# Optimization experiments

Measured on AMD Instinct MI355X. Metric: run time of the kernel, lower is better.

Reference implementation:

```python
import jax, jax.numpy as jnp
import numpy as np

B, D, L = 2, 1024, 4096   # batch, channels (= num_heads), seq len
FS = 4                    # filter_size
DEPTH = 11                # ceil(log2((L-1)/(FS-1)+1))
LN_EPS = 1e-5


def setup_inputs() -> dict:
    key = jax.random.key(0)
    ks = jax.random.split(key, 7)
    return {
        "x": jax.random.normal(ks[0], (B, D, L), jnp.float32),
        "h0": jax.random.normal(ks[1], (D, 1, FS), jnp.float32) * 0.2,
        "h1": jax.random.normal(ks[2], (D, 1, FS), jnp.float32) * 0.2,
        "w_mix": jax.random.normal(ks[3], (D, D), jnp.float32) / np.sqrt(D),
        "b_mix": jnp.zeros((D,), jnp.float32),
        "ln_gamma": jnp.ones((D,), jnp.float32),
        "ln_beta": jnp.zeros((D,), jnp.float32),
    }


def _dw_conv(a, h, dilation):
    # depthwise (groups = D) dilated conv1d, cross-correlation like torch
    return jax.lax.conv_general_dilated(
        a, h, window_strides=(1,), padding='VALID',
        rhs_dilation=(dilation,),
        dimension_numbers=('NCH', 'OIH', 'NCH'),
        feature_group_count=D)


def reference(x, h0, h1, w_mix, b_mix, ln_gamma, ln_beta):
    # --- multires conv tree ---
    a = x
    dilation = 1
    a_list, b_list = [], []
    for _ in range(DEPTH):
        pad = dilation * (FS - 1)
        ap = jnp.pad(a, ((0, 0), (0, 0), (pad, 0)))  # left causal pad
        b = _dw_conv(ap, h1, dilation)
        a = _dw_conv(ap, h0, dilation)
        a_list.append(a)
        b_list.append(b)
        dilation *= 2
    # --- gated combination across scales (deepest level first) ---
    a_rev = a_list[::-1]
    b_rev = b_list[::-1]
    y = jnp.zeros_like(x)
    gated = None
    for i in range(DEPTH):
        if i + 1 < DEPTH:
            gated = jax.nn.sigmoid(a_rev[i]) * b_rev[i + 1]
        # last iteration reuses the previous gated tensor (matches original)
        y = y + gated
    # --- 1x1 channel mix (Dropout1d is identity in eval) + residual ---
    mixed = jnp.einsum('oc,bcl->bol', w_mix, y) + b_mix[None, :, None]
    z = mixed + x
    # --- LayerNorm over channel dim ---
    mu = jnp.mean(z, axis=1, keepdims=True)
    var = jnp.mean(jnp.square(z - mu), axis=1, keepdims=True)
    out = (z - mu) * jax.lax.rsqrt(var + LN_EPS)
    out = out * ln_gamma[None, :, None] + ln_beta[None, :, None]
    return out
```

## Files before the change

### kernel.cpp

```cpp
#include <hip/hip_runtime.h>
#include <hip/hip_bf16.h>
#include <hip/hip_fp16.h>

#define NB 2
#define ND 1024
#define NL 4096
#define NFS 4
#define NDEPTH 11
#define LN_EPS 1e-5f

#define BM 128
#define BN 128
#define BK 32
#define NKI (ND / BK)
#define ASZ (BM * BK)

#define CPAD 3072
#define CBUF (CPAD + NL)

typedef __bf16 bf16x8 __attribute__((ext_vector_type(8)));
typedef float f32x4 __attribute__((ext_vector_type(4)));
typedef _Float16 half8 __attribute__((ext_vector_type(8)));

__device__ __forceinline__ unsigned short f2bf(float f) {
    __hip_bfloat16 h = __float2bfloat16(f);
    unsigned short u;
    __builtin_memcpy(&u, &h, 2);
    return u;
}

__device__ __forceinline__ float bf2f(unsigned short u) {
    unsigned int ui = (unsigned int)u << 16;
    float f;
    __builtin_memcpy(&f, &ui, 4);
    return f;
}

__device__ __forceinline__ unsigned int pack2bf(float lo, float hi) {
    return (unsigned int)f2bf(lo) | ((unsigned int)f2bf(hi) << 16);
}

__device__ __forceinline__ void llds16(const void* g, void* l) {
    __builtin_amdgcn_global_load_lds(
        (const __attribute__((address_space(1))) unsigned int*)g,
        (__attribute__((address_space(3))) unsigned int*)l, 16, 0, 0);
}

__global__ __launch_bounds__(256) void wconv_kernel(const float* __restrict__ w,
                                                    unsigned short* __restrict__ wbf) {
    const int idx8 = (blockIdx.x * 256 + threadIdx.x) * 8;
    const float4 v0 = *reinterpret_cast<const float4*>(w + idx8);
    const float4 v1 = *reinterpret_cast<const float4*>(w + idx8 + 4);
    uint4 o;
    o.x = pack2bf(v0.x, v0.y);
    o.y = pack2bf(v0.z, v0.w);
    o.z = pack2bf(v1.x, v1.y);
    o.w = pack2bf(v1.z, v1.w);
    *reinterpret_cast<uint4*>(wbf + idx8) = o;
}

__global__ __launch_bounds__(512, 8) void conv_cascade_kernel(const float* __restrict__ x,
                                                              const float* __restrict__ h0,
                                                              const float* __restrict__ h1,
                                                              unsigned short* __restrict__ ybf) {
    __shared__ _Float16 a_sh[2][CBUF];
    const int row = blockIdx.x;
    const int d = row & (ND - 1);
    const int t = threadIdx.x;

    if (t < CPAD / 8) {
        *reinterpret_cast<half8*>(&a_sh[0][t * 8]) = (half8)0;
        *reinterpret_cast<half8*>(&a_sh[1][t * 8]) = (half8)0;
    }

    const float* xrow = x + (size_t)row * NL;

    _Float16 h0c[NFS], h1c[NFS];
#pragma unroll
    for (int k = 0; k < NFS; ++k) {
        h0c[k] = (_Float16)h0[d * NFS + k];
        h1c[k] = (_Float16)h1[d * NFS + k];
    }

    const int A = CPAD + t * 8;
    half8 cur;
    {
        const float4 v0 = *reinterpret_cast<const float4*>(xrow + t * 8);
        const float4 v1 = *reinterpret_cast<const float4*>(xrow + t * 8 + 4);
        cur[0] = (_Float16)v0.x; cur[1] = (_Float16)v0.y;
        cur[2] = (_Float16)v0.z; cur[3] = (_Float16)v0.w;
        cur[4] = (_Float16)v1.x; cur[5] = (_Float16)v1.y;
        cur[6] = (_Float16)v1.z; cur[7] = (_Float16)v1.w;
    }
    _Float16* rbp = &a_sh[0][0];
    _Float16* wbp = &a_sh[1][0];
    *reinterpret_cast<half8*>(&rbp[A]) = cur;

    const __half2 nlog2e = __float2half2_rn(-1.44269504f);
    const __half2 one2 = __float2half2_rn(1.f);
    const __half2 two2 = __float2half2_rn(2.f);
    __half2 yacc2[4];
#pragma unroll
    for (int p = 0; p < 4; ++p) yacc2[p] = __float2half2_rn(0.f);
    half8 bprev = (half8)0;
    __syncthreads();

    half8 an, bn;

#define CMATH(a1, a2, a3)                                           \
    an = cur * h0c[3] + (a1)*h0c[2] + (a2)*h0c[1] + (a3)*h0c[0];    \
    bn = cur * h1c[3] + (a1)*h1c[2] + (a2)*h1c[1] + (a3)*h1c[0];

#define GATE(SC2)                                                   \
    {                                                               \
        __half2 ap[4], bp[4];                                       \
        __builtin_memcpy(ap, &an, 16);                              \
        __builtin_memcpy(bp, &bprev, 16);                           \
        _Pragma("unroll") for (int p = 0; p < 4; ++p) {             \
            const __half2 e = h2exp2(__hmul2(ap[p], nlog2e));       \
            const __half2 s = h2rcp(__hadd2(e, one2));              \
            const __half2 g = __hmul2(__hmul2(s, bp[p]), SC2);      \
            yacc2[p] = __hadd2(g, yacc2[p]);                        \
        }                                                           \
    }

#define CFIN()                                                      \
    {                                                               \
        *reinterpret_cast<half8*>(&wbp[A]) = an;                    \
        cur = an;                                                   \
        bprev = bn;                                                 \
        _Float16* tmpp = rbp; rbp = wbp; wbp = tmpp;                \
    }

    {
        const half8 m = *reinterpret_cast<const half8*>(&rbp[A - 8]);
        const half8 a1 = __builtin_shufflevector(m, cur, 7, 8, 9, 10, 11, 12, 13, 14);
        const half8 a2 = __builtin_shufflevector(m, cur, 6, 7, 8, 9, 10, 11, 12, 13);
        const half8 a3 = __builtin_shufflevector(m, cur, 5, 6, 7, 8, 9, 10, 11, 12);
        CMATH(a1, a2, a3)
        CFIN()
        __syncthreads();
    }

    {
        const half8 m = *reinterpret_cast<const half8*>(&rbp[A - 8]);
        const half8 a1 = __builtin_shufflevector(m, cur, 6, 7, 8, 9, 10, 11, 12, 13);
        const half8 a2 = __builtin_shufflevector(m, cur, 4, 5, 6, 7, 8, 9, 10, 11);
        const half8 a3 = __builtin_shufflevector(m, cur, 2, 3, 4, 5, 6, 7, 8, 9);
        CMATH(a1, a2, a3)
        GATE(two2)
        CFIN()
        __syncthreads();
    }

    {
        const half8 m = *reinterpret_cast<const half8*>(&rbp[A - 8]);
        const half8 m2 = *reinterpret_cast<const half8*>(&rbp[A - 16]);
        const half8 a1 = __builtin_shufflevector(m, cur, 4, 5, 6, 7, 8, 9, 10, 11);
        const half8 a3 = __builtin_shufflevector(m2, m, 4, 5, 6, 7, 8, 9, 10, 11);
        CMATH(a1, m, a3)
        GATE(one2)
        CFIN()
        __syncthreads();
    }

    int dil = 8;
#pragma unroll 1
    for (int lev = 3; lev <= 9; ++lev) {
        const half8 a1 = *reinterpret_cast<const half8*>(&rbp[A - dil]);
        const half8 a2 = *reinterpret_cast<const half8*>(&rbp[A - 2 * dil]);
        const half8 a3 = *reinterpret_cast<const half8*>(&rbp[A - 3 * dil]);
        CMATH(a1, a2, a3)
        GATE(one2)
        CFIN()
        dil <<= 1;
        __syncthreads();
    }

    {
        const half8 a1 = *reinterpret_cast<const half8*>(&rbp[A - 1024]);
        const half8 a2 = *reinterpret_cast<const half8*>(&rbp[A - 2048]);
        const half8 a3 = *reinterpret_cast<const half8*>(&rbp[A - 3072]);
        an = cur * h0c[3] + a1 * h0c[2] + a2 * h0c[1] + a3 * h0c[0];
        GATE(one2)
    }
#undef CMATH
#undef GATE
#undef CFIN

    const float2 f0 = __half22float2(yacc2[0]);
    const float2 f1 = __half22float2(yacc2[1]);
    const float2 f2 = __half22float2(yacc2[2]);
    const float2 f3 = __half22float2(yacc2[3]);
    uint4 o;
    o.x = pack2bf(f0.x, f0.y);
    o.y = pack2bf(f1.x, f1.y);
    o.z = pack2bf(f2.x, f2.y);
    o.w = pack2bf(f3.x, f3.y);
    *reinterpret_cast<uint4*>(ybf + (size_t)row * NL + t * 8) = o;
}

__global__ __launch_bounds__(256) void transpose_kernel(const unsigned short* __restrict__ ybf,
                                                        unsigned short* __restrict__ yT) {
    __shared__ unsigned short tile[64][66];
    const int l0 = blockIdx.x * 64;
    const int c0 = blockIdx.y * 64;
    const int b = blockIdx.z;
    const int t = threadIdx.x;
    const int li = t & 63, cg = t >> 6;
#pragma unroll
    for (int k = 0; k < 16; ++k) {
        const int ci = cg * 16 + k;
        tile[ci][li] = ybf[(size_t)(b * ND + c0 + ci) * NL + l0 + li];
    }
    __syncthreads();
    const int ci2 = t & 63, lg = t >> 6;
#pragma unroll
    for (int k = 0; k < 16; ++k) {
        const int li2 = lg * 16 + k;
        yT[((size_t)b * NL + l0 + li2) * ND + c0 + ci2] = tile[ci2][li2];
    }
}

__global__ __launch_bounds__(256) void gemm_kernel(const unsigned short* __restrict__ wbf,
                                                   const unsigned short* __restrict__ yT,
                                                   const float* __restrict__ bmix,
                                                   unsigned short* __restrict__ mixed) {
    __shared__ unsigned short As[3][BM][BK];
    __shared__ unsigned short Bs[3][BN][BK];

    const int orig = blockIdx.x;
    const int wgid = (orig & 7) * 64 + (orig >> 3);
    const int b = wgid & 1;
    const int m0 = ((wgid >> 1) & 7) * BM;
    const int n0 = (wgid >> 4) * BN;

    const int t = threadIdx.x;
    const int lane = t & 63, wid = t >> 6;
    const int wr = wid >> 1, wc = wid & 1;
    const int fr = lane & 15;
    const int fk = (lane >> 4) * 8;

    const int srow = wid * 32 + (lane >> 2);
    const int sk = (lane & 3) * 8;
    const unsigned short* Ag = wbf + (size_t)(m0 + srow) * ND + sk;
    const unsigned short* Bg = yT + ((size_t)b * NL + n0 + srow) * ND + sk;
    unsigned short* A0 = &As[0][0][0];
    unsigned short* B0 = &Bs[0][0][0];
    unsigned short* AsW = A0 + wid * 32 * BK;
    unsigned short* BsW = B0 + wid * 32 * BK;

#define STAGE(bo, kt)                           \
    llds16(Ag + (kt), AsW + (bo));              \
    llds16(Ag + (kt) + 16 * ND, AsW + (bo) + 16 * BK); \
    llds16(Bg + (kt), BsW + (bo));              \
    llds16(Bg + (kt) + 16 * ND, BsW + (bo) + 16 * BK);

    f32x4 acc[4][4];
#pragma unroll
    for (int mi = 0; mi < 4; ++mi)
#pragma unroll
        for (int ni = 0; ni < 4; ++ni)
            acc[mi][ni] = (f32x4){0.f, 0.f, 0.f, 0.f};

    STAGE(0, 0)
    STAGE(ASZ, BK)

    int bc = 0;
    int bs = 2;
#pragma unroll 1
    for (int ki = 0; ki < NKI; ++ki) {
        if (ki + 1 < NKI) {
            asm volatile("s_waitcnt vmcnt(4)" ::: "memory");
        } else {
            asm volatile("s_waitcnt vmcnt(0)" ::: "memory");
        }
        __builtin_amdgcn_s_barrier();
        __builtin_amdgcn_sched_barrier(0);

        if (ki + 2 < NKI) {
            const int bo = bs * ASZ;
            const int kt = (ki + 2) * BK;
            STAGE(bo, kt)
        }

        const int bco = bc * ASZ;
        bf16x8 af[4], bv[4];
#pragma unroll
        for (int mi = 0; mi < 4; ++mi)
            af[mi] = *reinterpret_cast<const bf16x8*>(A0 + bco + (wr * 64 + mi * 16 + fr) * BK + fk);
#pragma unroll
        for (int ni = 0; ni < 4; ++ni)
            bv[ni] = *reinterpret_cast<const bf16x8*>(B0 + bco + (wc * 64 + ni * 16 + fr) * BK + fk);
#pragma unroll
        for (int mi = 0; mi < 4; ++mi)
#pragma unroll
            for (int ni = 0; ni < 4; ++ni)
                acc[mi][ni] = __builtin_amdgcn_mfma_f32_16x16x32_bf16(af[mi], bv[ni],
                                                                      acc[mi][ni], 0, 0, 0);
        bc = (bc == 2) ? 0 : bc + 1;
        bs = (bs == 2) ? 0 : bs + 1;
    }
#undef STAGE

    const size_t bbase = (size_t)b * ND * NL;
#pragma unroll
    for (int mi = 0; mi < 4; ++mi) {
#pragma unroll
        for (int r = 0; r < 4; ++r) {
            const int o = m0 + wr * 64 + mi * 16 + (lane >> 4) * 4 + r;
            const float bm = bmix[o];
            const size_t rowbase = bbase + (size_t)o * NL;
#pragma unroll
            for (int ni = 0; ni < 4; ++ni) {
                const int l = n0 + wc * 64 + ni * 16 + fr;
                mixed[rowbase + l] = f2bf(acc[mi][ni][r] + bm);
            }
        }
    }
}

__global__ __launch_bounds__(512) void ln_kernel(const unsigned short* __restrict__ mixed,
                                                 const float* __restrict__ x,
                                                 const float* __restrict__ gamma,
                                                 const float* __restrict__ beta,
                                                 float* __restrict__ out) {
    const int b = blockIdx.y;
    const int l0 = blockIdx.x * 32;
    const int tl = threadIdx.x & 31, tg = threadIdx.x >> 5;
    const size_t base = (size_t)b * ND * NL + l0 + tl;

    float zv[64];
    float s = 0.f, q = 0.f;
#pragma unroll
    for (int j = 0; j < 64; ++j) {
        const size_t idx = base + (size_t)(tg + j * 16) * NL;
        const float v = bf2f(mixed[idx]) + x[idx];
        zv[j] = v;
        s += v;
        q += v * v;
    }

    __shared__ float sred[16][33], qred[16][33];
    __shared__ float mu_s[32], rs_s[32];
    sred[tg][tl] = s;
    qred[tg][tl] = q;
    __syncthreads();
    if (tg == 0) {
        float S = 0.f, Q = 0.f;
#pragma unroll
        for (int g = 0; g < 16; ++g) {
            S += sred[g][tl];
            Q += qred[g][tl];
        }
        const float mu = S * (1.f / ND);
        const float var = Q * (1.f / ND) - mu * mu;
        mu_s[tl] = mu;
        rs_s[tl] = rsqrtf(var + LN_EPS);
    }
    __syncthreads();
    const float mu = mu_s[tl], rs = rs_s[tl];
#pragma unroll
    for (int j = 0; j < 64; ++j) {
        const int c = tg + j * 16;
        out[base + (size_t)c * NL] = (zv[j] - mu) * rs * gamma[c] + beta[c];
    }
}

extern "C" void kernel_launch(void* const* d_in, const int* in_sizes, int n_in,
                              void* d_out, int out_size, void* d_ws, size_t ws_size,
                              hipStream_t stream) {
    (void)in_sizes; (void)n_in; (void)out_size; (void)ws_size;
    const float* x = (const float*)d_in[0];
    const float* h0 = (const float*)d_in[1];
    const float* h1 = (const float*)d_in[2];
    const float* wmix = (const float*)d_in[3];
    const float* bmix = (const float*)d_in[4];
    const float* gamma = (const float*)d_in[5];
    const float* beta = (const float*)d_in[6];
    float* out = (float*)d_out;

    char* ws = (char*)d_ws;
    unsigned short* ybf = (unsigned short*)(ws);
    unsigned short* yT = (unsigned short*)(ws + (size_t)16 * 1024 * 1024);
    unsigned short* wbf = (unsigned short*)(ws + (size_t)32 * 1024 * 1024);
    unsigned short* mixed = (unsigned short*)(ws + (size_t)34 * 1024 * 1024);

    wconv_kernel<<<dim3(ND * ND / (256 * 8)), 256, 0, stream>>>(wmix, wbf);
    conv_cascade_kernel<<<dim3(NB * ND), 512, 0, stream>>>(x, h0, h1, ybf);
    transpose_kernel<<<dim3(NL / 64, ND / 64, NB), 256, 0, stream>>>(ybf, yT);
    gemm_kernel<<<dim3(512), 256, 0, stream>>>(wbf, yT, bmix, mixed);
    ln_kernel<<<dim3(NL / 32, NB), 512, 0, stream>>>(mixed, x, gamma, beta, out);
}
```

Before: 99.98 us.

## Compute first three conv levels in registers from global x; widen LN blocks

The conv cascade now loads a 32-element halo of x directly from global memory and computes levels 0-2 entirely in registers. This removes three shared-memory round trips and three block barriers, at the cost of redundant halo loads and extra register pressure, and it drops the min-blocks launch bound. The LayerNorm kernel moves to 1024 threads per block with half as many values per thread, and caches gamma and beta in shared memory. That lowers per-thread register use but makes the reduction step wider.

```diff
diff --git a/kernel.cpp b/kernel.cpp
--- a/kernel.cpp
+++ b/kernel.cpp
@@ -44,6 +44,22 @@
     __builtin_amdgcn_global_load_lds(
         (const __attribute__((address_space(1))) unsigned int*)g,
         (__attribute__((address_space(3))) unsigned int*)l, 16, 0, 0);
+}
+
+__device__ __forceinline__ half8 ldx8(const float* p) {
+    const float4 v0 = *reinterpret_cast<const float4*>(p);
+    const float4 v1 = *reinterpret_cast<const float4*>(p + 4);
+    half8 r;
+    r[0] = (_Float16)v0.x; r[1] = (_Float16)v0.y;
+    r[2] = (_Float16)v0.z; r[3] = (_Float16)v0.w;
+    r[4] = (_Float16)v1.x; r[5] = (_Float16)v1.y;
+    r[6] = (_Float16)v1.z; r[7] = (_Float16)v1.w;
+    return r;
+}
+
+__device__ __forceinline__ half8 ldx8z(const float* xrow, int off) {
+    half8 v = ldx8(xrow + (off >= 0 ? off : 0));
+    return (off >= 0) ? v : (half8)0;
 }
 
 __global__ __launch_bounds__(256) void wconv_kernel(const float* __restrict__ w,
@@ -59,10 +75,10 @@
     *reinterpret_cast<uint4*>(wbf + idx8) = o;
 }
 
-__global__ __launch_bounds__(512, 8) void conv_cascade_kernel(const float* __restrict__ x,
-                                                              const float* __restrict__ h0,
-                                                              const float* __restrict__ h1,
-                                                              unsigned short* __restrict__ ybf) {
+__global__ __launch_bounds__(512) void conv_cascade_kernel(const float* __restrict__ x,
+                                                           const float* __restrict__ h0,
+                                                           const float* __restrict__ h1,
+                                                           unsigned short* __restrict__ ybf) {
     __shared__ _Float16 a_sh[2][CBUF];
     const int row = blockIdx.x;
     const int d = row & (ND - 1);
@@ -82,19 +98,14 @@
         h1c[k] = (_Float16)h1[d * NFS + k];
     }
 
-    const int A = CPAD + t * 8;
-    half8 cur;
-    {
-        const float4 v0 = *reinterpret_cast<const float4*>(xrow + t * 8);
-        const float4 v1 = *reinterpret_cast<const float4*>(xrow + t * 8 + 4);
-        cur[0] = (_Float16)v0.x; cur[1] = (_Float16)v0.y;
-        cur[2] = (_Float16)v0.z; cur[3] = (_Float16)v0.w;
-        cur[4] = (_Float16)v1.x; cur[5] = (_Float16)v1.y;
-        cur[6] = (_Float16)v1.z; cur[7] = (_Float16)v1.w;
-    }
-    _Float16* rbp = &a_sh[0][0];
-    _Float16* wbp = &a_sh[1][0];
-    *reinterpret_cast<half8*>(&rbp[A]) = cur;
+    const int l8 = t * 8;
+    const int A = CPAD + l8;
+
+    const half8 X0 = ldx8z(xrow, l8 - 32);
+    const half8 X1 = ldx8z(xrow, l8 - 24);
+    const half8 X2 = ldx8z(xrow, l8 - 16);
+    const half8 X3 = ldx8z(xrow, l8 - 8);
+    const half8 C  = ldx8(xrow + l8);
 
     const __half2 nlog2e = __float2half2_rn(-1.44269504f);
     const __half2 one2 = __float2half2_rn(1.f);
@@ -102,91 +113,95 @@
     __half2 yacc2[4];
 #pragma unroll
     for (int p = 0; p < 4; ++p) yacc2[p] = __float2half2_rn(0.f);
-    half8 bprev = (half8)0;
-    __syncthreads();
-
-    half8 an, bn;
-
-#define CMATH(a1, a2, a3)                                           \
-    an = cur * h0c[3] + (a1)*h0c[2] + (a2)*h0c[1] + (a3)*h0c[0];    \
-    bn = cur * h1c[3] + (a1)*h1c[2] + (a2)*h1c[1] + (a3)*h1c[0];
-
-#define GATE(SC2)                                                   \
+
+#define SH1(L, R) __builtin_shufflevector(L, R, 7, 8, 9, 10, 11, 12, 13, 14)
+#define SH2(L, R) __builtin_shufflevector(L, R, 6, 7, 8, 9, 10, 11, 12, 13)
+#define SH3(L, R) __builtin_shufflevector(L, R, 5, 6, 7, 8, 9, 10, 11, 12)
+#define SH4(L, R) __builtin_shufflevector(L, R, 4, 5, 6, 7, 8, 9, 10, 11)
+#define SH6(L, R) __builtin_shufflevector(L, R, 2, 3, 4, 5, 6, 7, 8, 9)
+#define CONV_D1(L, R, hc) ((R)*hc[3] + SH1(L, R) * hc[2] + SH2(L, R) * hc[1] + SH3(L, R) * hc[0])
+#define CONV_D2(L, R, hc) ((R)*hc[3] + SH2(L, R) * hc[2] + SH4(L, R) * hc[1] + SH6(L, R) * hc[0])
+
+#define GATE(av, bv, SC2)                                           \
     {                                                               \
-        __half2 ap[4], bp[4];                                       \
-        __builtin_memcpy(ap, &an, 16);                              \
-        __builtin_memcpy(bp, &bprev, 16);                           \
+        __half2 ap_[4], bp_[4];                                     \
+        __builtin_memcpy(ap_, &(av), 16);                           \
+        __builtin_memcpy(bp_, &(bv), 16);                           \
         _Pragma("unroll") for (int p = 0; p < 4; ++p) {             \
-            const __half2 e = h2exp2(__hmul2(ap[p], nlog2e));       \
+            const __half2 e = h2exp2(__hmul2(ap_[p], nlog2e));      \
             const __half2 s = h2rcp(__hadd2(e, one2));              \
-            const __half2 g = __hmul2(__hmul2(s, bp[p]), SC2);      \
+            const __half2 g = __hmul2(__hmul2(s, bp_[p]), SC2);     \
             yacc2[p] = __hadd2(g, yacc2[p]);                        \
         }                                                           \
     }
 
-#define CFIN()                                                      \
-    {                                                               \
-        *reinterpret_cast<half8*>(&wbp[A]) = an;                    \
-        cur = an;                                                   \
-        bprev = bn;                                                 \
-        _Float16* tmpp = rbp; rbp = wbp; wbp = tmpp;                \
-    }
-
-    {
-        const half8 m = *reinterpret_cast<const half8*>(&rbp[A - 8]);
-        const half8 a1 = __builtin_shufflevector(m, cur, 7, 8, 9, 10, 11, 12, 13, 14);
-        const half8 a2 = __builtin_shufflevector(m, cur, 6, 7, 8, 9, 10, 11, 12, 13);
-        const half8 a3 = __builtin_shufflevector(m, cur, 5, 6, 7, 8, 9, 10, 11, 12);
-        CMATH(a1, a2, a3)
-        CFIN()
-        __syncthreads();
-    }
-
-    {
-        const half8 m = *reinterpret_cast<const half8*>(&rbp[A - 8]);
-        const half8 a1 = __builtin_shufflevector(m, cur, 6, 7, 8, 9, 10, 11, 12, 13);
-        const half8 a2 = __builtin_shufflevector(m, cur, 4, 5, 6, 7, 8, 9, 10, 11);
-        const half8 a3 = __builtin_shufflevector(m, cur, 2, 3, 4, 5, 6, 7, 8, 9);
-        CMATH(a1, a2, a3)
-        GATE(two2)
-        CFIN()
-        __syncthreads();
-    }
-
-    {
-        const half8 m = *reinterpret_cast<const half8*>(&rbp[A - 8]);
-        const half8 m2 = *reinterpret_cast<const half8*>(&rbp[A - 16]);
-        const half8 a1 = __builtin_shufflevector(m, cur, 4, 5, 6, 7, 8, 9, 10, 11);
-        const half8 a3 = __builtin_shufflevector(m2, m, 4, 5, 6, 7, 8, 9, 10, 11);
-        CMATH(a1, m, a3)
-        GATE(one2)
-        CFIN()
-        __syncthreads();
+    const half8 a0_1 = CONV_D1(X0, X1, h0c);
+    const half8 a0_2 = CONV_D1(X1, X2, h0c);
+    const half8 a0_3 = CONV_D1(X2, X3, h0c);
+    const half8 a0_4 = CONV_D1(X3, C, h0c);
+    const half8 b0 = CONV_D1(X3, C, h1c);
+
+    const half8 a1_2 = CONV_D2(a0_1, a0_2, h0c);
+    const half8 a1_3 = CONV_D2(a0_2, a0_3, h0c);
+    const half8 a1_4 = CONV_D2(a0_3, a0_4, h0c);
+    const half8 b1 = CONV_D2(a0_3, a0_4, h1c);
+    GATE(a1_4, b0, two2)
+
+    const half8 s4 = SH4(a1_3, a1_4);
+    const half8 s12 = SH4(a1_2, a1_3);
+    const half8 a2 = a1_4 * h0c[3] + s4 * h0c[2] + a1_3 * h0c[1] + s12 * h0c[0];
+    const half8 b2 = a1_4 * h1c[3] + s4 * h1c[2] + a1_3 * h1c[1] + s12 * h1c[0];
+    GATE(a2, b1, one2)
+
+    half8 cur = a2;
+    half8 bprev = b2;
+    _Float16* rbp = &a_sh[0][0];
+    _Float16* wbp = &a_sh[1][0];
+    *reinterpret_cast<half8*>(&rbp[A]) = cur;
+    __syncthreads();
+
+    half8 an, bn;
+#define CMATH(a1v, a2v, a3v)                                              \
+    an = cur * h0c[3] + (a1v)*h0c[2] + (a2v)*h0c[1] + (a3v)*h0c[0];       \
+    bn = cur * h1c[3] + (a1v)*h1c[2] + (a2v)*h1c[1] + (a3v)*h1c[0];
+#define CFIN()                                                            \
+    {                                                                     \
+        *reinterpret_cast<half8*>(&wbp[A]) = an;                          \
+        cur = an;                                                         \
+        bprev = bn;                                                       \
+        _Float16* tmpp = rbp; rbp = wbp; wbp = tmpp;                      \
     }
 
     int dil = 8;
 #pragma unroll 1
     for (int lev = 3; lev <= 9; ++lev) {
-        const half8 a1 = *reinterpret_cast<const half8*>(&rbp[A - dil]);
-        const half8 a2 = *reinterpret_cast<const half8*>(&rbp[A - 2 * dil]);
-        const half8 a3 = *reinterpret_cast<const half8*>(&rbp[A - 3 * dil]);
-        CMATH(a1, a2, a3)
-        GATE(one2)
+        const half8 a1v = *reinterpret_cast<const half8*>(&rbp[A - dil]);
+        const half8 a2v = *reinterpret_cast<const half8*>(&rbp[A - 2 * dil]);
+        const half8 a3v = *reinterpret_cast<const half8*>(&rbp[A - 3 * dil]);
+        CMATH(a1v, a2v, a3v)
+        GATE(an, bprev, one2)
         CFIN()
         dil <<= 1;
         __syncthreads();
     }
 
     {
-        const half8 a1 = *reinterpret_cast<const half8*>(&rbp[A - 1024]);
-        const half8 a2 = *reinterpret_cast<const half8*>(&rbp[A - 2048]);
-        const half8 a3 = *reinterpret_cast<const half8*>(&rbp[A - 3072]);
-        an = cur * h0c[3] + a1 * h0c[2] + a2 * h0c[1] + a3 * h0c[0];
-        GATE(one2)
+        const half8 a1v = *reinterpret_cast<const half8*>(&rbp[A - 1024]);
+        const half8 a2v = *reinterpret_cast<const half8*>(&rbp[A - 2048]);
+        const half8 a3v = *reinterpret_cast<const half8*>(&rbp[A - 3072]);
+        an = cur * h0c[3] + a1v * h0c[2] + a2v * h0c[1] + a3v * h0c[0];
+        GATE(an, bprev, one2)
     }
 #undef CMATH
 #undef GATE
 #undef CFIN
+#undef CONV_D1
+#undef CONV_D2
+#undef SH1
+#undef SH2
+#undef SH3
+#undef SH4
+#undef SH6
 
     const float2 f0 = __half22float2(yacc2[0]);
     const float2 f1 = __half22float2(yacc2[1]);
@@ -320,36 +335,42 @@
     }
 }
 
-__global__ __launch_bounds__(512) void ln_kernel(const unsigned short* __restrict__ mixed,
-                                                 const float* __restrict__ x,
-                                                 const float* __restrict__ gamma,
-                                                 const float* __restrict__ beta,
-                                                 float* __restrict__ out) {
+__global__ __launch_bounds__(1024) void ln_kernel(const unsigned short* __restrict__ mixed,
+                                                  const float* __restrict__ x,
+                                                  const float* __restrict__ gamma,
+                                                  const float* __restrict__ beta,
+                                                  float* __restrict__ out) {
+    __shared__ float gsh[ND], bsh[ND];
+    __shared__ float sred[32][33], qred[32][33];
+    __shared__ float mu_s[32], rs_s[32];
+
+    const int t = threadIdx.x;
+    gsh[t] = gamma[t];
+    bsh[t] = beta[t];
+
     const int b = blockIdx.y;
     const int l0 = blockIdx.x * 32;
-    const int tl = threadIdx.x & 31, tg = threadIdx.x >> 5;
+    const int tl = t & 31, tg = t >> 5;
     const size_t base = (size_t)b * ND * NL + l0 + tl;
 
-    float zv[64];
+    float zv[32];
     float s = 0.f, q = 0.f;
 #pragma unroll
-    for (int j = 0; j < 64; ++j) {
-        const size_t idx = base + (size_t)(tg + j * 16) * NL;
+    for (int j = 0; j < 32; ++j) {
+        const size_t idx = base + (size_t)(tg + j * 32) * NL;
         const float v = bf2f(mixed[idx]) + x[idx];
         zv[j] = v;
         s += v;
         q += v * v;
     }
 
-    __shared__ float sred[16][33], qred[16][33];
-    __shared__ float mu_s[32], rs_s[32];
     sred[tg][tl] = s;
     qred[tg][tl] = q;
     __syncthreads();
     if (tg == 0) {
         float S = 0.f, Q = 0.f;
 #pragma unroll
-        for (int g = 0; g < 16; ++g) {
+        for (int g = 0; g < 32; ++g) {
             S += sred[g][tl];
             Q += qred[g][tl];
         }
@@ -361,9 +382,9 @@
     __syncthreads();
     const float mu = mu_s[tl], rs = rs_s[tl];
 #pragma unroll
-    for (int j = 0; j < 64; ++j) {
-        const int c = tg + j * 16;
-        out[base + (size_t)c * NL] = (zv[j] - mu) * rs * gamma[c] + beta[c];
+    for (int j = 0; j < 32; ++j) {
+        const int c = tg + j * 32;
+        out[base + (size_t)c * NL] = (zv[j] - mu) * rs * gsh[c] + bsh[c];
     }
 }
 
@@ -390,5 +411,5 @@
     conv_cascade_kernel<<<dim3(NB * ND), 512, 0, stream>>>(x, h0, h1, ybf);
     transpose_kernel<<<dim3(NL / 64, ND / 64, NB), 256, 0, stream>>>(ybf, yT);
     gemm_kernel<<<dim3(512), 256, 0, stream>>>(wbf, yT, bmix, mixed);
-    ln_kernel<<<dim3(NL / 32, NB), 512, 0, stream>>>(mixed, x, gamma, beta, out);
-}
+    ln_kernel<<<dim3(NL / 32, NB), 1024, 0, stream>>>(mixed, x, gamma, beta, out);
+}
```

Result: faster. 93.26 us (-6.7%).
